# Kernel optimization log

Measured on AMD Instinct MI355X. Metric: run time of the kernel, lower is better.

The kernel has to match this reference:

```python
import jax, jax.numpy as jnp
import numpy as np

DIM = 4096
BLOCK = 64  # power of 2
B, S = 8, 4096


def _hadamard(n: int) -> np.ndarray:
    # Sylvester construction; matches the natural-order FWHT butterfly.
    H = np.array([[1.0]], dtype=np.float32)
    base = np.array([[1.0, 1.0], [1.0, -1.0]], dtype=np.float32)
    while H.shape[0] < n:
        H = np.kron(H, base)
    return H


def setup_inputs() -> dict:
    key = jax.random.key(0)
    kx, ks1, ks2, kp = jax.random.split(key, 4)
    x = jax.random.normal(kx, (B, S, DIM), dtype=jnp.float32)
    sign1 = (jax.random.bernoulli(ks1, 0.5, (DIM,)).astype(jnp.float32) * 2.0 - 1.0)
    sign2 = (jax.random.bernoulli(ks2, 0.5, (DIM,)).astype(jnp.float32) * 2.0 - 1.0)
    perm = jax.random.permutation(kp, DIM).astype(jnp.int32)
    return {"x": x, "sign1": sign1, "sign2": sign2, "perm": perm}


def reference(x, sign1, sign2, perm):
    # Block Hadamard: y = (x reshaped into blocks) @ H / sqrt(block)
    # The sequential butterfly in the torch code computes exactly H_sylvester @ v.
    H = jnp.asarray(_hadamard(BLOCK)) / jnp.sqrt(jnp.float32(BLOCK))  # [block, block]
    *lead, d = x.shape
    nb = d // BLOCK
    h = x.reshape(*lead, nb, BLOCK)
    h = jnp.einsum('...i,ij->...j', h, H)  # H is symmetric, so order is irrelevant
    y = h.reshape(*lead, d)
    # DPD: diag(sign1) -> permutation -> diag(sign2)
    y = y * sign1
    y = y[..., perm]
    y = y * sign2
    return y
```

## Files before the change

kernel.cpp:

```cpp
#include <hip/hip_runtime.h>


constexpr int DIM = 4096;
constexpr int TPB = 256;
constexpr int EPT = DIM / TPB;

__global__ __launch_bounds__(TPB)
void bh_dpd_kernel(const float* __restrict__ x,
                   const float* __restrict__ sign1,
                   const float* __restrict__ sign2,
                   const int*   __restrict__ perm,
                   float* __restrict__ out)
{
    __shared__ float h[DIM];

    const int t = threadIdx.x;
    const long long row = blockIdx.x;
    const float* xr   = x   + row * (long long)DIM;
    float*       outr = out + row * (long long)DIM;

    const int base = t * EPT;

    float v[EPT];
    {
        const float4* xv = reinterpret_cast<const float4*>(xr + base);
        #pragma unroll
        for (int j = 0; j < EPT / 4; ++j) {
            float4 a = xv[j];
            v[j*4+0] = a.x; v[j*4+1] = a.y; v[j*4+2] = a.z; v[j*4+3] = a.w;
        }
    }

    #pragma unroll
    for (int s = 1; s <= 8; s <<= 1) {
        #pragma unroll
        for (int i = 0; i < EPT; ++i) {
            if ((i & s) == 0) {
                float a = v[i], b = v[i + s];
                v[i]     = a + b;
                v[i + s] = a - b;
            }
        }
    }
    #pragma unroll
    for (int i = 0; i < EPT; ++i) {
        float p = __shfl_xor(v[i], 1, 64);
        v[i] = (t & 1) ? (p - v[i]) : (v[i] + p);
    }
    #pragma unroll
    for (int i = 0; i < EPT; ++i) {
        float p = __shfl_xor(v[i], 2, 64);
        v[i] = (t & 2) ? (p - v[i]) : (v[i] + p);
    }

    {
        const float4* s1v = reinterpret_cast<const float4*>(sign1 + base);
        float4* hv = reinterpret_cast<float4*>(h + base);
        #pragma unroll
        for (int j = 0; j < EPT / 4; ++j) {
            float4 s = s1v[j];
            float4 o;
            o.x = v[j*4+0] * 0.125f * s.x;
            o.y = v[j*4+1] * 0.125f * s.y;
            o.z = v[j*4+2] * 0.125f * s.z;
            o.w = v[j*4+3] * 0.125f * s.w;
            hv[j] = o;
        }
    }
    __syncthreads();

    {
        const int4*   pv  = reinterpret_cast<const int4*>(perm  + base);
        const float4* s2v = reinterpret_cast<const float4*>(sign2 + base);
        float4* ov = reinterpret_cast<float4*>(outr + base);
        #pragma unroll
        for (int j = 0; j < EPT / 4; ++j) {
            int4   p = pv[j];
            float4 s = s2v[j];
            float4 o;
            o.x = h[p.x] * s.x;
            o.y = h[p.y] * s.y;
            o.z = h[p.z] * s.z;
            o.w = h[p.w] * s.w;
            ov[j] = o;
        }
    }
}

extern "C" void kernel_launch(void* const* d_in, const int* in_sizes, int n_in,
                              void* d_out, int out_size, void* d_ws, size_t ws_size,
                              hipStream_t stream) {
    const float* x     = (const float*)d_in[0];
    const float* sign1 = (const float*)d_in[1];
    const float* sign2 = (const float*)d_in[2];
    const int*   perm  = (const int*)d_in[3];
    float* out = (float*)d_out;

    const int rows = out_size / DIM;
    bh_dpd_kernel<<<dim3(rows), dim3(TPB), 0, stream>>>(x, sign1, sign2, perm, out);
}
```

Baseline: 938.2 us.

## Switch to coalesced strided float4 layout with shuffle-based Hadamard stages

Each thread now loads four float4 groups at stride 1024 floats instead of one contiguous 16-float chunk, so each wavefront's loads and stores are fully coalesced. The 64-point Hadamard is split into a 4-point in-register butterfly followed by four cross-lane shuffle stages. Global loads of x and stores of out are nontemporal. The cost is more shuffle instructions (16 per group per stage) in place of register-only butterflies.

New measurement: 843.6 us. 1.11x faster.

```diff
diff --git a/kernel.cpp b/kernel.cpp
--- a/kernel.cpp
+++ b/kernel.cpp
@@ -3,7 +3,10 @@
 
 constexpr int DIM = 4096;
 constexpr int TPB = 256;
-constexpr int EPT = DIM / TPB;
+constexpr int NG  = DIM / (TPB * 4);
+
+typedef float f32x4 __attribute__((ext_vector_type(4)));
+typedef int   i32x4 __attribute__((ext_vector_type(4)));
 
 __global__ __launch_bounds__(TPB)
 void bh_dpd_kernel(const float* __restrict__ x,
@@ -15,75 +18,65 @@
     __shared__ float h[DIM];
 
     const int t = threadIdx.x;
+    const int l = t & 63;
     const long long row = blockIdx.x;
     const float* xr   = x   + row * (long long)DIM;
     float*       outr = out + row * (long long)DIM;
 
-    const int base = t * EPT;
+    f32x4 g[NG];
+    #pragma unroll
+    for (int j = 0; j < NG; ++j) {
+        const f32x4* src = reinterpret_cast<const f32x4*>(xr + j * 1024) + t;
+        g[j] = __builtin_nontemporal_load(src);
+    }
 
-    float v[EPT];
-    {
-        const float4* xv = reinterpret_cast<const float4*>(xr + base);
+    #pragma unroll
+    for (int j = 0; j < NG; ++j) {
+        float a0 = g[j].x, a1 = g[j].y, a2 = g[j].z, a3 = g[j].w;
+        float b0 = a0 + a1, b1 = a0 - a1;
+        float b2 = a2 + a3, b3 = a2 - a3;
+        g[j].x = b0 + b2; g[j].y = b1 + b3;
+        g[j].z = b0 - b2; g[j].w = b1 - b3;
+    }
+
+    #pragma unroll
+    for (int m = 1; m <= 8; m <<= 1) {
+        const bool hi = (l & m) != 0;
         #pragma unroll
-        for (int j = 0; j < EPT / 4; ++j) {
-            float4 a = xv[j];
-            v[j*4+0] = a.x; v[j*4+1] = a.y; v[j*4+2] = a.z; v[j*4+3] = a.w;
+        for (int j = 0; j < NG; ++j) {
+            float px = __shfl_xor(g[j].x, m, 64);
+            float py = __shfl_xor(g[j].y, m, 64);
+            float pz = __shfl_xor(g[j].z, m, 64);
+            float pw = __shfl_xor(g[j].w, m, 64);
+            g[j].x = hi ? (px - g[j].x) : (g[j].x + px);
+            g[j].y = hi ? (py - g[j].y) : (g[j].y + py);
+            g[j].z = hi ? (pz - g[j].z) : (g[j].z + pz);
+            g[j].w = hi ? (pw - g[j].w) : (g[j].w + pw);
         }
     }
 
     #pragma unroll
-    for (int s = 1; s <= 8; s <<= 1) {
-        #pragma unroll
-        for (int i = 0; i < EPT; ++i) {
-            if ((i & s) == 0) {
-                float a = v[i], b = v[i + s];
-                v[i]     = a + b;
-                v[i + s] = a - b;
-            }
-        }
-    }
-    #pragma unroll
-    for (int i = 0; i < EPT; ++i) {
-        float p = __shfl_xor(v[i], 1, 64);
-        v[i] = (t & 1) ? (p - v[i]) : (v[i] + p);
-    }
-    #pragma unroll
-    for (int i = 0; i < EPT; ++i) {
-        float p = __shfl_xor(v[i], 2, 64);
-        v[i] = (t & 2) ? (p - v[i]) : (v[i] + p);
-    }
-
-    {
-        const float4* s1v = reinterpret_cast<const float4*>(sign1 + base);
-        float4* hv = reinterpret_cast<float4*>(h + base);
-        #pragma unroll
-        for (int j = 0; j < EPT / 4; ++j) {
-            float4 s = s1v[j];
-            float4 o;
-            o.x = v[j*4+0] * 0.125f * s.x;
-            o.y = v[j*4+1] * 0.125f * s.y;
-            o.z = v[j*4+2] * 0.125f * s.z;
-            o.w = v[j*4+3] * 0.125f * s.w;
-            hv[j] = o;
-        }
+    for (int j = 0; j < NG; ++j) {
+        f32x4 s = reinterpret_cast<const f32x4*>(sign1 + j * 1024)[t];
+        f32x4 o;
+        o.x = g[j].x * 0.125f * s.x;
+        o.y = g[j].y * 0.125f * s.y;
+        o.z = g[j].z * 0.125f * s.z;
+        o.w = g[j].w * 0.125f * s.w;
+        reinterpret_cast<f32x4*>(h + j * 1024)[t] = o;
     }
     __syncthreads();
 
-    {
-        const int4*   pv  = reinterpret_cast<const int4*>(perm  + base);
-        const float4* s2v = reinterpret_cast<const float4*>(sign2 + base);
-        float4* ov = reinterpret_cast<float4*>(outr + base);
-        #pragma unroll
-        for (int j = 0; j < EPT / 4; ++j) {
-            int4   p = pv[j];
-            float4 s = s2v[j];
-            float4 o;
-            o.x = h[p.x] * s.x;
-            o.y = h[p.y] * s.y;
-            o.z = h[p.z] * s.z;
-            o.w = h[p.w] * s.w;
-            ov[j] = o;
-        }
+    #pragma unroll
+    for (int j = 0; j < NG; ++j) {
+        i32x4 p = reinterpret_cast<const i32x4*>(perm + j * 1024)[t];
+        f32x4 s = reinterpret_cast<const f32x4*>(sign2 + j * 1024)[t];
+        f32x4 o;
+        o.x = h[p.x] * s.x;
+        o.y = h[p.y] * s.y;
+        o.z = h[p.z] * s.z;
+        o.w = h[p.w] * s.w;
+        __builtin_nontemporal_store(o, reinterpret_cast<f32x4*>(outr + j * 1024) + t);
     }
 }
 
```
